# Kernel optimization log

Hardware: AMD Instinct MI355X
Metric: run time of the kernel (lower is better)

## Reference

```python
import jax, jax.numpy as jnp
import numpy as np

B, S, C, NH = 4, 2048, 1024, 16
HD = C // NH


def setup_inputs() -> dict:
    key = jax.random.key(0)
    ks = jax.random.split(key, 8)
    w = lambda k, shape: (jax.random.normal(k, shape, dtype=jnp.float32) * 0.02)
    return {
        "x": jax.random.normal(ks[0], (B, S, C), dtype=jnp.float32),
        "y": jax.random.normal(ks[1], (B, S, C), dtype=jnp.float32),
        "mask": jnp.zeros((B, S), dtype=bool),  # True = padded key
        "Wq_w": w(ks[2], (C, C)),
        "Wq_b": jnp.zeros((C,), dtype=jnp.float32),
        "Wkv_w": w(ks[3], (2 * C, C)),
        "Wkv_b": jnp.zeros((2 * C,), dtype=jnp.float32),
        "Wo_w": w(ks[4], (C, C)),
        "Wo_b": jnp.zeros((C,), dtype=jnp.float32),
    }


def reference(x, y, mask, Wq_w, Wq_b, Wkv_w, Wkv_b, Wo_w, Wo_b):
    b, s, c = x.shape
    # projections (torch nn.Linear: x @ W.T + b)
    q = (x @ Wq_w.T + Wq_b).reshape(b, s, NH, HD).transpose(0, 2, 1, 3)  # bhsd
    kv = (y @ Wkv_w.T + Wkv_b).reshape(b, s, 2, NH, HD)
    k = kv[:, :, 0].transpose(0, 2, 1, 3)  # bhsd
    v = kv[:, :, 1].transpose(0, 2, 1, 3)  # bhsd
    # scores: [b, h, s_q, s_k]
    attn = jnp.einsum("bhqd,bhkd->bhqk", q, k) / np.sqrt(HD).astype(np.float32)
    causal = jnp.triu(jnp.ones((s, s), dtype=bool), 1)  # True above diagonal
    combined = causal[None, None] | mask[:, None, None, :]
    attn = jnp.where(combined, -jnp.inf, attn)
    attn = jax.nn.softmax(attn, axis=-1)
    out = jnp.einsum("bhqk,bhkd->bhqd", attn, v)
    out = out.transpose(0, 2, 1, 3).reshape(b, s, c)
    return out @ Wo_w.T + Wo_b
```

## Files before the change

kernel.cpp:

```cpp
#include <hip/hip_runtime.h>
#include <stdint.h>

#define B_  4
#define S_  2048
#define C_  1024
#define NH_ 16
#define HD_ 64
#define M_  (B_*S_)
#define NT_ (S_/64)

typedef __attribute__((ext_vector_type(8))) short bf16x8;
typedef __attribute__((ext_vector_type(4))) float f32x4;

typedef __attribute__((address_space(1))) const unsigned int gu32;
typedef __attribute__((address_space(3))) unsigned int lu32;

__device__ __forceinline__ void gload16(const void* g, void* l) {
    __builtin_amdgcn_global_load_lds((gu32*)g, (lu32*)l, 16, 0, 0);
}

__device__ __forceinline__ unsigned short f2bf(float f) {
    union { float f; unsigned u; } v; v.f = f;
    unsigned r = v.u + 0x7FFF + ((v.u >> 16) & 1);
    return (unsigned short)(r >> 16);
}

__global__ __launch_bounds__(256)
void cvt_all(const float4* __restrict__ x, const float4* __restrict__ y,
             const float4* __restrict__ wq, const float4* __restrict__ wkv,
             const float4* __restrict__ wo,
             uint4* __restrict__ xb, uint4* __restrict__ yb, uint4* __restrict__ wqb,
             uint4* __restrict__ wkvb, uint4* __restrict__ wob) {
    int i = blockIdx.x * 256 + threadIdx.x;
    const float4* src; uint4* dst; int off;
    if      (i < 1048576) { src = x;   dst = xb;   off = i; }
    else if (i < 2097152) { src = y;   dst = yb;   off = i - 1048576; }
    else if (i < 2228224) { src = wq;  dst = wqb;  off = i - 2097152; }
    else if (i < 2490368) { src = wkv; dst = wkvb; off = i - 2228224; }
    else                  { src = wo;  dst = wob;  off = i - 2490368; }
    float4 a = src[2*off], b = src[2*off+1];
    union { unsigned short s[8]; uint4 v; } u;
    u.s[0]=f2bf(a.x); u.s[1]=f2bf(a.y); u.s[2]=f2bf(a.z); u.s[3]=f2bf(a.w);
    u.s[4]=f2bf(b.x); u.s[5]=f2bf(b.y); u.s[6]=f2bf(b.z); u.s[7]=f2bf(b.w);
    dst[off] = u.v;
}

#define BM 128
#define BN 128
#define BK 64

template<int MODE>
__device__ __forceinline__
void gemm_body(const unsigned short* __restrict__ A, const unsigned short* __restrict__ Bt,
               const float* __restrict__ bias,
               unsigned short* __restrict__ out0, unsigned short* __restrict__ out1,
               float* __restrict__ outf, int K, int N, int bx, int by,
               unsigned short* As, unsigned short* Bs)
{
    int t = threadIdx.x;
    int lane = t & 63, w = t >> 6;
    int wx = w & 1, wy = w >> 1;
    int quad = lane >> 4, l16 = lane & 15;

    f32x4 acc[4][4] = {};
    int rowA = by * BM, rowB = bx * BN;
    int lr = lane >> 3;
    int lc = (lane & 7) * 8;
    const unsigned short* gA = A  + (size_t)(rowA + w*32 + lr)*K + lc;
    const unsigned short* gB = Bt + (size_t)(rowB + w*32 + lr)*K + lc;
    unsigned short* lA = &As[(w*32)*BK];
    unsigned short* lB = &Bs[(w*32)*BK];

    for (int kb = 0; kb < K; kb += BK) {
        #pragma unroll
        for (int i = 0; i < 4; ++i) {
            gload16(gA + (size_t)i*8*K + kb, lA + i*8*BK);
            gload16(gB + (size_t)i*8*K + kb, lB + i*8*BK);
        }
        asm volatile("s_waitcnt vmcnt(0)" ::: "memory");
        __syncthreads();
        #pragma unroll
        for (int ks = 0; ks < 2; ++ks) {
            bf16x8 af[4], bfr[4];
            #pragma unroll
            for (int mt = 0; mt < 4; ++mt)
                af[mt] = *reinterpret_cast<const bf16x8*>(&As[(wy*64 + mt*16 + l16)*BK + ks*32 + quad*8]);
            #pragma unroll
            for (int nt = 0; nt < 4; ++nt)
                bfr[nt] = *reinterpret_cast<const bf16x8*>(&Bs[(wx*64 + nt*16 + l16)*BK + ks*32 + quad*8]);
            #pragma unroll
            for (int mt = 0; mt < 4; ++mt)
                #pragma unroll
                for (int nt = 0; nt < 4; ++nt)
                    acc[mt][nt] = __builtin_amdgcn_mfma_f32_16x16x32_bf16(af[mt], bfr[nt], acc[mt][nt], 0, 0, 0);
        }
        __syncthreads();
    }

    const float QSCALE = 0.180336880111f;
    #pragma unroll
    for (int mt = 0; mt < 4; ++mt) {
        #pragma unroll
        for (int nt = 0; nt < 4; ++nt) {
            int gn = bx*BN + wx*64 + nt*16 + l16;
            float bv = bias[gn];
            #pragma unroll
            for (int r = 0; r < 4; ++r) {
                int gm = by*BM + wy*64 + mt*16 + quad*4 + r;
                float v = acc[mt][nt][r] + bv;
                if (MODE == 2) {
                    outf[(size_t)gm * N + gn] = v;
                } else if (MODE == 0) {
                    v *= QSCALE;
                    int b = gm >> 11, s = gm & 2047;
                    int h = gn >> 6,  d = gn & 63;
                    out0[(((size_t)(b*NH_ + h)*S_ + s) << 6) + d] = f2bf(v);
                } else {
                    int b = gm >> 11, s = gm & 2047;
                    if (gn < C_) {
                        int h = gn >> 6, d = gn & 63;
                        out0[(((size_t)(b*NH_ + h)*S_ + s) << 6) + d] = f2bf(v);
                    } else {
                        int n2 = gn - C_;
                        int h = n2 >> 6, d = n2 & 63;
                        out1[((size_t)(b*NH_ + h)*HD_ + d)*S_ + s] = f2bf(v);
                    }
                }
            }
        }
    }
}

__global__ __launch_bounds__(256)
void proj_fused(const unsigned short* __restrict__ xb, const unsigned short* __restrict__ Wqb,
                const float* __restrict__ Wq_b,
                const unsigned short* __restrict__ yb, const unsigned short* __restrict__ Wkvb,
                const float* __restrict__ Wkv_b,
                unsigned short* __restrict__ Qg, unsigned short* __restrict__ Kg,
                unsigned short* __restrict__ Vt)
{
    __shared__ unsigned short As[BM*BK];
    __shared__ unsigned short Bs[BN*BK];
    int id = blockIdx.x;
    if (id < 512) {
        gemm_body<0>(xb, Wqb, Wq_b, Qg, nullptr, nullptr, C_, C_, id & 7, id >> 3, As, Bs);
    } else {
        int j = id - 512;
        gemm_body<1>(yb, Wkvb, Wkv_b, Kg, Vt, nullptr, C_, 2*C_, j & 15, j >> 4, As, Bs);
    }
}

__global__ __launch_bounds__(256)
void gemm_oproj(const unsigned short* __restrict__ A, const unsigned short* __restrict__ Bt,
                const float* __restrict__ bias, float* __restrict__ outf)
{
    __shared__ unsigned short As[BM*BK];
    __shared__ unsigned short Bs[BN*BK];
    gemm_body<2>(A, Bt, bias, nullptr, nullptr, outf, C_, C_, blockIdx.x, blockIdx.y, As, Bs);
}

__global__ __launch_bounds__(256, 4)
void attn_kernel(const unsigned short* __restrict__ Qg, const unsigned short* __restrict__ Kg,
                 const unsigned short* __restrict__ Vt, const unsigned char* __restrict__ maskp,
                 unsigned short* __restrict__ att)
{
    __shared__ unsigned short Pl[64*72];
    __shared__ float Lbuf[4][64];
    __shared__ float Linv[64];
    int t = threadIdx.x, lane = t & 63, w = t >> 6;
    int quad = lane >> 4, l16 = lane & 15;
    int bh = blockIdx.x, b = bh >> 4, h = bh & 15;
    int qi = blockIdx.y;

    const unsigned short* kbase = Kg + ((size_t)bh*S_ + w*16 + l16)*HD_ + quad*8;
    const unsigned short* vbase = Vt + ((size_t)bh*HD_ + w*16 + l16)*S_ + quad*8;
    int kp_row = w*16 + quad*4;
    const unsigned char* mbase = maskp + (size_t)b*S_ + kp_row;

    for (int half = 0; half < 2; ++half) {
        int qt = half ? (NT_ - 1 - qi) : qi;

        bf16x8 qf[4][2];
        #pragma unroll
        for (int m = 0; m < 4; ++m) {
            const unsigned short* qp = Qg + ((size_t)bh*S_ + qt*64 + m*16 + l16)*HD_;
            qf[m][0] = *reinterpret_cast<const bf16x8*>(qp + quad*8);
            qf[m][1] = *reinterpret_cast<const bf16x8*>(qp + 32 + quad*8);
        }
        f32x4 oacc[4] = {};
        float lsum[4] = {0.f, 0.f, 0.f, 0.f};

        bf16x8 kc0 = *reinterpret_cast<const bf16x8*>(kbase);
        bf16x8 kc1 = *reinterpret_cast<const bf16x8*>(kbase + 32);

        for (int kt = 0; kt <= qt; ++kt) {
            int ktn = (kt < qt) ? kt + 1 : kt;
            const unsigned short* kpn = kbase + (size_t)ktn*64*HD_;
            bf16x8 kn0 = *reinterpret_cast<const bf16x8*>(kpn);
            bf16x8 kn1 = *reinterpret_cast<const bf16x8*>(kpn + 32);
            const unsigned short* vp = vbase + kt*64;
            bf16x8 vc0 = *reinterpret_cast<const bf16x8*>(vp);
            bf16x8 vc1 = *reinterpret_cast<const bf16x8*>(vp + 32);

            unsigned m4 = *reinterpret_cast<const unsigned*>(mbase + kt*64);

            f32x4 sacc[4];
            #pragma unroll
            for (int m = 0; m < 4; ++m) {
                sacc[m] = __builtin_amdgcn_mfma_f32_16x16x32_bf16(kc0, qf[m][0], f32x4{}, 0, 0, 0);
                sacc[m] = __builtin_amdgcn_mfma_f32_16x16x32_bf16(kc1, qf[m][1], sacc[m], 0, 0, 0);
            }

            bool diag = (kt == qt);
            #pragma unroll
            for (int m = 0; m < 4; ++m) {
                float p[4];
                if (diag) {
                    #pragma unroll
                    for (int r = 0; r < 4; ++r) {
                        float s = sacc[m][r];
                        if (kp_row + r > m*16 + l16) s = -1e30f;
                        p[r] = __builtin_amdgcn_exp2f(s);
                    }
                } else {
                    #pragma unroll
                    for (int r = 0; r < 4; ++r)
                        p[r] = __builtin_amdgcn_exp2f(sacc[m][r]);
                }
                if (m4) {
                    #pragma unroll
                    for (int r = 0; r < 4; ++r)
                        if ((m4 >> (8*r)) & 0xFFu) p[r] = 0.f;
                }
                lsum[m] += (p[0] + p[1]) + (p[2] + p[3]);
                unsigned a01 = __builtin_amdgcn_perm(__float_as_uint(p[1]), __float_as_uint(p[0]), 0x07060302u);
                unsigned a23 = __builtin_amdgcn_perm(__float_as_uint(p[3]), __float_as_uint(p[2]), 0x07060302u);
                *reinterpret_cast<uint2*>(&Pl[(m*16 + l16)*72 + w*16 + quad*4]) = make_uint2(a01, a23);
            }
            __syncthreads();
            #pragma unroll
            for (int m = 0; m < 4; ++m) {
                bf16x8 pf0 = *reinterpret_cast<const bf16x8*>(&Pl[(m*16 + l16)*72 + quad*8]);
                bf16x8 pf1 = *reinterpret_cast<const bf16x8*>(&Pl[(m*16 + l16)*72 + 32 + quad*8]);
                oacc[m] = __builtin_amdgcn_mfma_f32_16x16x32_bf16(pf0, vc0, oacc[m], 0, 0, 0);
                oacc[m] = __builtin_amdgcn_mfma_f32_16x16x32_bf16(pf1, vc1, oacc[m], 0, 0, 0);
            }
            __syncthreads();
            kc0 = kn0; kc1 = kn1;
        }

        #pragma unroll
        for (int m = 0; m < 4; ++m) {
            lsum[m] += __shfl_xor(lsum[m], 16, 64);
            lsum[m] += __shfl_xor(lsum[m], 32, 64);
            Lbuf[w][m*16 + l16] = lsum[m];
        }
        __syncthreads();
        int q64 = t & 63;
        Linv[q64] = 1.0f / (Lbuf[0][q64] + Lbuf[1][q64] + Lbuf[2][q64] + Lbuf[3][q64]);
        __syncthreads();
        #pragma unroll
        for (int m = 0; m < 4; ++m) {
            #pragma unroll
            for (int r = 0; r < 4; ++r) {
                float iv = Linv[m*16 + quad*4 + r];
                int q = qt*64 + m*16 + quad*4 + r;
                att[((size_t)(b*S_ + q))*C_ + h*HD_ + w*16 + l16] = f2bf(oacc[m][r] * iv);
            }
        }
        __syncthreads();
    }
}

extern "C" void kernel_launch(void* const* d_in, const int* in_sizes, int n_in,
                              void* d_out, int out_size, void* d_ws, size_t ws_size,
                              hipStream_t stream) {
    const float* x     = (const float*)d_in[0];
    const float* y     = (const float*)d_in[1];
    const unsigned char* mask = (const unsigned char*)d_in[2];
    const float* Wq_w  = (const float*)d_in[3];
    const float* Wq_b  = (const float*)d_in[4];
    const float* Wkv_w = (const float*)d_in[5];
    const float* Wkv_b = (const float*)d_in[6];
    const float* Wo_w  = (const float*)d_in[7];
    const float* Wo_b  = (const float*)d_in[8];
    float* out = (float*)d_out;

    unsigned short* xb   = (unsigned short*)d_ws;
    unsigned short* yb   = xb   + (size_t)M_*C_;
    unsigned short* Wqb  = yb   + (size_t)M_*C_;
    unsigned short* Wkvb = Wqb  + (size_t)C_*C_;
    unsigned short* Wob  = Wkvb + (size_t)2*C_*C_;
    unsigned short* Qg   = Wob  + (size_t)C_*C_;
    unsigned short* Kg   = Qg   + (size_t)M_*C_;
    unsigned short* Vtg  = Kg   + (size_t)M_*C_;
    unsigned short* att  = xb;

    cvt_all<<<10240, 256, 0, stream>>>((const float4*)x, (const float4*)y,
        (const float4*)Wq_w, (const float4*)Wkv_w, (const float4*)Wo_w,
        (uint4*)xb, (uint4*)yb, (uint4*)Wqb, (uint4*)Wkvb, (uint4*)Wob);

    proj_fused<<<1536, 256, 0, stream>>>(xb, Wqb, Wq_b, yb, Wkvb, Wkv_b, Qg, Kg, Vtg);
    attn_kernel<<<dim3(B_*NH_, NT_/2), 256, 0, stream>>>(Qg, Kg, Vtg, mask, att);
    gemm_oproj<<<dim3(C_/BN, M_/BM), 256, 0, stream>>>(att, Wob, Wo_b, out);
}
```

Before: 334.0 us.

## Replace projection GEMMs with 256x256 double-buffered swizzled-LDS pipelined kernel

Swaps the 128x128 single-buffered GEMM used by the QKV and output projections for a 256x256 tile kernel with 512 threads and 128KB of dynamic LDS. The next K-tile is prefetched into a second buffer while MFMAs run in four phases, with fine-grained vmcnt waits, barriers and setprio. An XOR swizzle on LDS columns is meant to cut bank conflicts. The goal is to hide global-load latency and raise data reuse per block. The cost is fewer blocks (128 for the output projection) and more LDS per block, so occupancy drops and wave quantization across CUs gets worse.

```diff
diff --git a/kernel.cpp b/kernel.cpp
--- a/kernel.cpp
+++ b/kernel.cpp
@@ -8,6 +8,7 @@
 #define HD_ 64
 #define M_  (B_*S_)
 #define NT_ (S_/64)
+#define NKT 16
 
 typedef __attribute__((ext_vector_type(8))) short bf16x8;
 typedef __attribute__((ext_vector_type(4))) float f32x4;
@@ -45,71 +46,134 @@
     dst[off] = u.v;
 }
 
-#define BM 128
-#define BN 128
-#define BK 64
+
+#define STAGE_A(mi, kb, db) do { \
+    gload16(gA + (size_t)(mi)*64*1024 + (kb),           sh + (db)*32768 + (w*8 + (mi)*64)*64); \
+    gload16(gA + ((size_t)(mi)*64 + 128)*1024 + (kb),   sh + (db)*32768 + (w*8 + 128 + (mi)*64)*64); \
+} while (0)
+
+#define STAGE_B(ni, kb, db) do { \
+    gload16(gB + (size_t)(ni)*32*1024 + (kb),           sh + (db)*32768 + 16384 + ((w>>2)*64 + (w&3)*8 + (ni)*32)*64); \
+    gload16(gB + ((size_t)(ni)*32 + 128)*1024 + (kb),   sh + (db)*32768 + 16384 + ((w>>2)*64 + (w&3)*8 + (ni)*32 + 128)*64); \
+} while (0)
 
 template<int MODE>
 __device__ __forceinline__
-void gemm_body(const unsigned short* __restrict__ A, const unsigned short* __restrict__ Bt,
-               const float* __restrict__ bias,
-               unsigned short* __restrict__ out0, unsigned short* __restrict__ out1,
-               float* __restrict__ outf, int K, int N, int bx, int by,
-               unsigned short* As, unsigned short* Bs)
+void gemm256_body(const unsigned short* __restrict__ A, const unsigned short* __restrict__ Bt,
+                  const float* __restrict__ bias,
+                  unsigned short* __restrict__ out0, unsigned short* __restrict__ out1,
+                  float* __restrict__ outf, int bx, int by, unsigned short* sh)
 {
-    int t = threadIdx.x;
-    int lane = t & 63, w = t >> 6;
-    int wx = w & 1, wy = w >> 1;
-    int quad = lane >> 4, l16 = lane & 15;
-
-    f32x4 acc[4][4] = {};
-    int rowA = by * BM, rowB = bx * BN;
-    int lr = lane >> 3;
-    int lc = (lane & 7) * 8;
-    const unsigned short* gA = A  + (size_t)(rowA + w*32 + lr)*K + lc;
-    const unsigned short* gB = Bt + (size_t)(rowB + w*32 + lr)*K + lc;
-    unsigned short* lA = &As[(w*32)*BK];
-    unsigned short* lB = &Bs[(w*32)*BK];
-
-    for (int kb = 0; kb < K; kb += BK) {
-        #pragma unroll
-        for (int i = 0; i < 4; ++i) {
-            gload16(gA + (size_t)i*8*K + kb, lA + i*8*BK);
-            gload16(gB + (size_t)i*8*K + kb, lB + i*8*BK);
-        }
-        asm volatile("s_waitcnt vmcnt(0)" ::: "memory");
-        __syncthreads();
-        #pragma unroll
-        for (int ks = 0; ks < 2; ++ks) {
-            bf16x8 af[4], bfr[4];
-            #pragma unroll
-            for (int mt = 0; mt < 4; ++mt)
-                af[mt] = *reinterpret_cast<const bf16x8*>(&As[(wy*64 + mt*16 + l16)*BK + ks*32 + quad*8]);
-            #pragma unroll
-            for (int nt = 0; nt < 4; ++nt)
-                bfr[nt] = *reinterpret_cast<const bf16x8*>(&Bs[(wx*64 + nt*16 + l16)*BK + ks*32 + quad*8]);
-            #pragma unroll
-            for (int mt = 0; mt < 4; ++mt)
-                #pragma unroll
-                for (int nt = 0; nt < 4; ++nt)
-                    acc[mt][nt] = __builtin_amdgcn_mfma_f32_16x16x32_bf16(af[mt], bfr[nt], acc[mt][nt], 0, 0, 0);
-        }
-        __syncthreads();
+    const int t = threadIdx.x;
+    const int lane = t & 63, w = t >> 6;
+    const int quad = lane >> 4, l16 = lane & 15;
+    const int wy = w >> 2, wx = w & 3;
+    const int s7 = l16 & 7;
+    const int colb = (quad ^ s7) << 3;
+    const int c16 = (lane & 7) ^ (lane >> 3);
+
+    const int rowA0 = by * 256;
+    const int colB0 = bx * 256;
+
+    const unsigned short* gA = A  + (size_t)(rowA0 + w*8 + (lane>>3))*1024 + c16*8;
+    const unsigned short* gB = Bt + (size_t)(colB0 + (w>>2)*64 + (w&3)*8 + (lane>>3))*1024 + c16*8;
+
+    f32x4 acc[2][2][4][2] = {};
+    bf16x8 af[4][2], bfv[2][2][2];
+
+    STAGE_A(0, 0, 0); STAGE_B(0, 0, 0); STAGE_B(1, 0, 0); STAGE_A(1, 0, 0);
+    asm volatile("s_waitcnt vmcnt(4)" ::: "memory");
+    __builtin_amdgcn_s_barrier();
+    __builtin_amdgcn_sched_barrier(0);
+
+    #pragma unroll 1
+    for (int kt = 0; kt < NKT; ++kt) {
+        const int cur = kt & 1;
+        const int dstb = cur ^ 1;
+        const unsigned short* Asb = sh + cur*32768;
+        const unsigned short* Bsb = Asb + 16384;
+        const int nkb = (kt + 1) * 64;
+        const bool pre = (kt + 1 < NKT);
+
+        #pragma unroll
+        for (int p = 0; p < 4; ++p) {
+            const int mi = p >> 1;
+            const int ni = (p & 1) ^ mi;
+
+            if (pre) {
+                if      (p == 0) STAGE_A(0, nkb, dstb);
+                else if (p == 1) STAGE_B(0, nkb, dstb);
+                else if (p == 2) STAGE_B(1, nkb, dstb);
+                else             STAGE_A(1, nkb, dstb);
+            }
+            if (p == 0) {
+                #pragma unroll
+                for (int mf = 0; mf < 4; ++mf) {
+                    int idx = (wy*128 + mf*16 + l16)*64 + colb;
+                    af[mf][0] = *(const bf16x8*)&Asb[idx];
+                    af[mf][1] = *(const bf16x8*)&Asb[idx ^ 32];
+                }
+                #pragma unroll
+                for (int nf = 0; nf < 2; ++nf) {
+                    int idx = (wx*64 + nf*16 + l16)*64 + colb;
+                    bfv[0][nf][0] = *(const bf16x8*)&Bsb[idx];
+                    bfv[0][nf][1] = *(const bf16x8*)&Bsb[idx ^ 32];
+                }
+            } else if (p == 1) {
+                #pragma unroll
+                for (int nf = 0; nf < 2; ++nf) {
+                    int idx = (wx*64 + 32 + nf*16 + l16)*64 + colb;
+                    bfv[1][nf][0] = *(const bf16x8*)&Bsb[idx];
+                    bfv[1][nf][1] = *(const bf16x8*)&Bsb[idx ^ 32];
+                }
+            } else if (p == 2) {
+                #pragma unroll
+                for (int mf = 0; mf < 4; ++mf) {
+                    int idx = (wy*128 + 64 + mf*16 + l16)*64 + colb;
+                    af[mf][0] = *(const bf16x8*)&Asb[idx];
+                    af[mf][1] = *(const bf16x8*)&Asb[idx ^ 32];
+                }
+            }
+
+            __builtin_amdgcn_s_barrier();
+            __builtin_amdgcn_s_setprio(1);
+            #pragma unroll
+            for (int mf = 0; mf < 4; ++mf)
+                #pragma unroll
+                for (int nf = 0; nf < 2; ++nf) {
+                    acc[mi][ni][mf][nf] = __builtin_amdgcn_mfma_f32_16x16x32_bf16(af[mf][0], bfv[ni][nf][0], acc[mi][ni][mf][nf], 0, 0, 0);
+                    acc[mi][ni][mf][nf] = __builtin_amdgcn_mfma_f32_16x16x32_bf16(af[mf][1], bfv[ni][nf][1], acc[mi][ni][mf][nf], 0, 0, 0);
+                }
+            __builtin_amdgcn_s_setprio(0);
+
+            if (p == 0) {
+                if (pre) asm volatile("s_waitcnt vmcnt(2)" ::: "memory");
+                else     asm volatile("s_waitcnt vmcnt(0)" ::: "memory");
+            } else if (p == 3 && pre) {
+                asm volatile("s_waitcnt vmcnt(4)" ::: "memory");
+            }
+            __builtin_amdgcn_s_barrier();
+            __builtin_amdgcn_sched_barrier(0);
+        }
     }
 
     const float QSCALE = 0.180336880111f;
     #pragma unroll
-    for (int mt = 0; mt < 4; ++mt) {
-        #pragma unroll
-        for (int nt = 0; nt < 4; ++nt) {
-            int gn = bx*BN + wx*64 + nt*16 + l16;
-            float bv = bias[gn];
+    for (int mi = 0; mi < 2; ++mi)
+    #pragma unroll
+    for (int ni = 0; ni < 2; ++ni)
+    #pragma unroll
+    for (int nf = 0; nf < 2; ++nf) {
+        int gn = colB0 + wx*64 + ni*32 + nf*16 + l16;
+        float bv = bias[gn];
+        #pragma unroll
+        for (int mf = 0; mf < 4; ++mf) {
             #pragma unroll
             for (int r = 0; r < 4; ++r) {
-                int gm = by*BM + wy*64 + mt*16 + quad*4 + r;
-                float v = acc[mt][nt][r] + bv;
+                int gm = rowA0 + wy*128 + mi*64 + mf*16 + quad*4 + r;
+                float v = acc[mi][ni][mf][nf][r] + bv;
                 if (MODE == 2) {
-                    outf[(size_t)gm * N + gn] = v;
+                    outf[(size_t)gm * 1024 + gn] = v;
                 } else if (MODE == 0) {
                     v *= QSCALE;
                     int b = gm >> 11, s = gm & 2047;
@@ -131,32 +195,30 @@
     }
 }
 
-__global__ __launch_bounds__(256)
-void proj_fused(const unsigned short* __restrict__ xb, const unsigned short* __restrict__ Wqb,
-                const float* __restrict__ Wq_b,
-                const unsigned short* __restrict__ yb, const unsigned short* __restrict__ Wkvb,
-                const float* __restrict__ Wkv_b,
-                unsigned short* __restrict__ Qg, unsigned short* __restrict__ Kg,
-                unsigned short* __restrict__ Vt)
+__global__ __launch_bounds__(512, 2)
+void proj_fused256(const unsigned short* __restrict__ xb, const unsigned short* __restrict__ Wqb,
+                   const float* __restrict__ Wq_b,
+                   const unsigned short* __restrict__ yb, const unsigned short* __restrict__ Wkvb,
+                   const float* __restrict__ Wkv_b,
+                   unsigned short* __restrict__ Qg, unsigned short* __restrict__ Kg,
+                   unsigned short* __restrict__ Vt)
 {
-    __shared__ unsigned short As[BM*BK];
-    __shared__ unsigned short Bs[BN*BK];
+    extern __shared__ unsigned short sh[];
     int id = blockIdx.x;
-    if (id < 512) {
-        gemm_body<0>(xb, Wqb, Wq_b, Qg, nullptr, nullptr, C_, C_, id & 7, id >> 3, As, Bs);
+    if (id < 128) {
+        gemm256_body<0>(xb, Wqb, Wq_b, Qg, nullptr, nullptr, id & 3, id >> 2, sh);
     } else {
-        int j = id - 512;
-        gemm_body<1>(yb, Wkvb, Wkv_b, Kg, Vt, nullptr, C_, 2*C_, j & 15, j >> 4, As, Bs);
+        int j = id - 128;
+        gemm256_body<1>(yb, Wkvb, Wkv_b, Kg, Vt, nullptr, j & 7, j >> 3, sh);
     }
 }
 
-__global__ __launch_bounds__(256)
-void gemm_oproj(const unsigned short* __restrict__ A, const unsigned short* __restrict__ Bt,
-                const float* __restrict__ bias, float* __restrict__ outf)
+__global__ __launch_bounds__(512, 2)
+void gemm_oproj256(const unsigned short* __restrict__ A, const unsigned short* __restrict__ Bt,
+                   const float* __restrict__ bias, float* __restrict__ outf)
 {
-    __shared__ unsigned short As[BM*BK];
-    __shared__ unsigned short Bs[BN*BK];
-    gemm_body<2>(A, Bt, bias, nullptr, nullptr, outf, C_, C_, blockIdx.x, blockIdx.y, As, Bs);
+    extern __shared__ unsigned short sh[];
+    gemm256_body<2>(A, Bt, bias, nullptr, nullptr, outf, blockIdx.x & 3, blockIdx.x >> 2, sh);
 }
 
 __global__ __launch_bounds__(256, 4)
@@ -296,11 +358,18 @@
     unsigned short* Vtg  = Kg   + (size_t)M_*C_;
     unsigned short* att  = xb;
 
+    static bool once = []() {
+        hipFuncSetAttribute((const void*)proj_fused256, hipFuncAttributeMaxDynamicSharedMemorySize, 131072);
+        hipFuncSetAttribute((const void*)gemm_oproj256, hipFuncAttributeMaxDynamicSharedMemorySize, 131072);
+        return true;
+    }();
+    (void)once;
+
     cvt_all<<<10240, 256, 0, stream>>>((const float4*)x, (const float4*)y,
         (const float4*)Wq_w, (const float4*)Wkv_w, (const float4*)Wo_w,
         (uint4*)xb, (uint4*)yb, (uint4*)Wqb, (uint4*)Wkvb, (uint4*)Wob);
 
-    proj_fused<<<1536, 256, 0, stream>>>(xb, Wqb, Wq_b, yb, Wkvb, Wkv_b, Qg, Kg, Vtg);
+    proj_fused256<<<384, 512, 131072, stream>>>(xb, Wqb, Wq_b, yb, Wkvb, Wkv_b, Qg, Kg, Vtg);
     attn_kernel<<<dim3(B_*NH_, NT_/2), 256, 0, stream>>>(Qg, Kg, Vtg, mask, att);
-    gemm_oproj<<<dim3(C_/BN, M_/BM), 256, 0, stream>>>(att, Wob, Wo_b, out);
-}
+    gemm_oproj256<<<128, 512, 131072, stream>>>(att, Wob, Wo_b, out);
+}
```

Result: no change. 334.3 us (+0.1%).
